# Kernel tuning notes

Measured on AMD Instinct MI355X. Metric: run time of the kernel, lower is better.

## Reference

```python
import jax, jax.numpy as jnp
import numpy as np

NEG_SLOPE = 0.2
EPS = 1e-6
K = 16


def vec_lna(x, Wf, Wd):
    # x: (B, Cin, 3, ...). Vector-neuron linear + VN-LeakyReLU.
    p = jnp.einsum('oc,bc...->bo...', Wf, x)          # features (B, Cout, 3, ...)
    d = jnp.einsum('oc,bc...->bo...', Wd, x)          # directions (B, Cd, 3, ...), Cd=Cout or 1 (shared)
    dot = jnp.sum(p * d, axis=2, keepdims=True)
    dsq = jnp.sum(d * d, axis=2, keepdims=True)
    p_ref = p - (dot / (dsq + EPS)) * d               # reflect negative part onto hyperplane
    return NEG_SLOPE * p + (1.0 - NEG_SLOPE) * jnp.where(dot >= 0, p, p_ref)


def knn_idx_fn(pts, k):
    # pts: (B, N, 3) -> (B, N, k) indices of k nearest neighbors (incl. self)
    sq = jnp.sum(pts * pts, axis=-1)                  # (B, N)
    d2 = sq[:, :, None] + sq[:, None, :] - 2.0 * jnp.einsum('bnd,bmd->bnm', pts, pts)
    _, idx = jax.lax.top_k(-d2, k)                    # smallest distances
    return idx


def graph_feature(x, idx):
    # x: (B, C, 3, N), idx: (B, N, k) -> (B, 2C, 3, N, k)
    nb = jax.vmap(lambda xb, ib: xb[:, :, ib])(x, idx)  # (B, C, 3, N, k)
    xc = x[..., None]
    return jnp.concatenate([nb - xc, jnp.broadcast_to(xc, nb.shape)], axis=1)


def _winit(key, co, ci):
    return jax.random.normal(key, (co, ci), dtype=jnp.float32) * np.sqrt(2.0 / ci).astype(np.float32)


def setup_inputs() -> dict:
    key = jax.random.key(0)
    ks = jax.random.split(key, 16)
    B, N = 4, 2048
    x = jax.random.normal(ks[0], (B, 3, N), dtype=jnp.float32)
    return {
        'x': x,
        'w1f': _winit(ks[1], 16, 2),   'w1d': _winit(ks[2], 16, 2),
        'w2f': _winit(ks[3], 32, 32),  'w2d': _winit(ks[4], 32, 32),
        'w3f': _winit(ks[5], 64, 64),  'w3d': _winit(ks[6], 64, 64),
        'w4f': _winit(ks[7], 128, 128),'w4d': _winit(ks[8], 128, 128),
        'wcf': _winit(ks[9], 128, 240),'wcd': _winit(ks[10], 1, 240),   # shared nonlinearity -> 1 dir channel
        'wi1f': _winit(ks[11], 128, 256), 'wi1d': _winit(ks[12], 128, 256),
        'wi2f': _winit(ks[13], 256, 128), 'wi2d': _winit(ks[14], 256, 128),
    }


def reference(x, w1f, w1d, w2f, w2d, w3f, w3d, w4f, w4d, wcf, wcd, wi1f, wi1d, wi2f, wi2d):
    # x: (B, 3, N)
    pts = jnp.transpose(x, (0, 2, 1))                 # (B, N, 3)
    idx = knn_idx_fn(pts, K)                          # (B, N, K) -- fixed graph (use_dg=False)
    h = x[:, None]                                    # (B, 1, 3, N)
    h = vec_lna(graph_feature(h, idx), w1f, w1d)
    x1 = h.mean(axis=-1)                              # (B, 16, 3, N)
    h = vec_lna(graph_feature(x1, idx), w2f, w2d)
    x2 = h.mean(axis=-1)                              # (B, 32, 3, N)
    h = vec_lna(graph_feature(x2, idx), w3f, w3d)
    x3 = h.mean(axis=-1)                              # (B, 64, 3, N)
    h = vec_lna(graph_feature(x3, idx), w4f, w4d)
    x4 = h.mean(axis=-1)                              # (B, 128, 3, N)
    xc = vec_lna(jnp.concatenate([x1, x2, x3, x4], axis=1), wcf, wcd)  # (B, 128, 3, N)
    xm = jnp.broadcast_to(xc.mean(axis=-1, keepdims=True), xc.shape)
    xcat = jnp.concatenate([xc, xm], axis=1)          # (B, 256, 3, N)
    x0 = vec_lna(vec_lna(xcat, wi1f, wi1d), wi2f, wi2d)
    inv = jnp.sum(xcat * x0, axis=2)                  # (B, 256, N) rotation-invariant features
    return inv
```

## Files before the change

kernel.cpp:

```cpp
#include <hip/hip_runtime.h>
#include <hip/hip_fp16.h>

#define NPTS  2048
#define BATCH 4
#define NBP   8192
#define MROWS 24576
#define KNN_K 16

typedef short bf16x8 __attribute__((ext_vector_type(8)));
typedef float f32x4  __attribute__((ext_vector_type(4)));

static __device__ __forceinline__ void split_bf16(float a, unsigned short& h, unsigned short& l)
{
    unsigned u = __float_as_uint(a);
    unsigned hr = (u + 0x7FFFu + ((u >> 16) & 1u)) & 0xFFFF0000u;
    h = (unsigned short)(hr >> 16);
    float rem = a - __uint_as_float(hr);
    unsigned v = __float_as_uint(rem);
    l = (unsigned short)((v + 0x7FFFu + ((v >> 16) & 1u)) >> 16);
}

static __device__ __forceinline__ float bf2(unsigned short h, unsigned short l)
{
    return __uint_as_float((unsigned)h << 16) + __uint_as_float((unsigned)l << 16);
// ... 144 lines not shown
        int v = row % 3;
        int gp = row / 3;
        int b = gp >> 11;
        int n = gp & (NPTS - 1);
        float xv = x[(b * 3 + v) * NPTS + n];
        float wv = wbig_val(w1f, w1d, o, 0, 16, 1);
        float val = xv * wv;
        if (o < 32) AH[(size_t)row * 32 + o] = __float2half(val);
        else        AG[(size_t)row * 32 + o - 32] = val;
    } else if (i < PC6) {
        float v = 0.f;
        unsigned short *ph, *pl;
        int ix;
        if (i < PC1) {
            ix = i - PC0;
            int c = ix & 31, j = ix >> 5;
            if (c < 16) v = wbig_val(w2f, w2d, j, c, 32, 16);
            ph = Wb2h; pl = Wb2l;
        } else if (i < PC2) {
            ix = i - PC1;
            int c = ix & 31, j = ix >> 5;
            v = wbig_val(w3f, w3d, j, c, 64, 32);
            ph = Wb3h; pl = Wb3l;
        } else if (i < PC3) {
            ix = i - PC2;
            int c = ix & 63, j = ix >> 6;
            v = wbig_val(w4f, w4d, j, c, 128, 64);
            ph = Wb4h; pl = Wb4l;
        } else if (i < PC4) {
            ix = i - PC3;
            int c = ix & 255, r = ix >> 8;
            if (c < 240) {
                if (r < 128) v = wcf[r * 240 + c];
                else if (r < 129) v = wcd[(r - 128) * 240 + c];
            }
            ph = Wch; pl = Wcl;
        } else if (i < PC5) {
            ix = i - PC4;
            int c = ix & 255, r = ix >> 8;
            if (r < 128) v = wi1f[r * 256 + c];
            else v = wi1d[(r - 128) * 256 + c];
            ph = Wi1h; pl = Wi1l;
        } else {
            ix = i - PC5;
            int c = ix & 127, r = ix >> 7;
            int o = r >> 1;
            v = (r & 1) ? wi2d[o * 128 + c] : wi2f[o * 128 + c];
            ph = Wi2h; pl = Wi2l;
        }
        unsigned short h, l;
        split_bf16(v, h, l);
        ph[ix] = h; pl[ix] = l;
    }
}

template <int OIN, int NF>
__global__ __launch_bounds__(256, 3) void edge_gemm_kernel(
    const __half* __restrict__ AHin, const float* __restrict__ AGin,
    const int* __restrict__ idx,
    unsigned short* __restrict__ X240h, unsigned short* __restrict__ X240l, int ooff,
    const unsigned short* __restrict__ Wh, const unsigned short* __restrict__ Wl,
    __half* __restrict__ OUTA, float* __restrict__ OUTG)
{
    constexpr int PTS = 16;
    constexpr int NC = NF * 64;
    constexpr int twoO = NC / 2;
    constexpr int LDW = 40;
    constexpr int CPT = OIN / 16;
    constexpr int twoOin = 2 * OIN;

    __shared__ unsigned short Xsh[48][32];
    __shared__ unsigned short Xsl[48][32];
    __shared__ unsigned short wbh[NC][LDW];
    __shared__ unsigned short wbl[NC][LDW];
    __shared__ int sIdx[PTS][KNN_K];

    const int lb = xcd_swizzle(blockIdx.x, gridDim.x);
    const int tid = threadIdx.x;

    for (int rr = tid; rr < NC; rr += 256) {
#pragma unroll
        for (int scc = 0; scc < 4; scc++) {
            *(uint4*)&wbh[rr][scc * 8] = *(const uint4*)(Wh + (size_t)rr * 32 + scc * 8);
            *(uint4*)&wbl[rr][scc * 8] = *(const uint4*)(Wl + (size_t)rr * 32 + scc * 8);
        }
    }
    for (int j = tid; j < PTS * KNN_K; j += 256)
        sIdx[j >> 4][j & 15] = idx[(lb * PTS + (j >> 4)) * KNN_K + (j & 15)];
    __syncthreads();

    const int op = tid & 15;
    const int pt = tid >> 4;
    const int gp = lb * PTS + pt;
    const int b = gp >> 11;
    const int rown = gp * 3;
    const int bbase = (b << 11) * 3;

    float cg[3][2 * CPT];
#pragma unroll
    for (int v = 0; v < 3; v++) {
        if constexpr (CPT == 2) {
            float4 c4 = *(const float4*)&AGin[(size_t)(rown + v) * twoOin + 4 * op];
            cg[v][0] = c4.x; cg[v][1] = c4.y; cg[v][2] = c4.z; cg[v][3] = c4.w;
        } else {
            float2 c2 = *(const float2*)&AGin[(size_t)(rown + v) * twoOin + 2 * op];
            cg[v][0] = c2.x; cg[v][1] = c2.y;
        }
    }
    float am[CPT][3];
#pragma unroll
    for (int c0 = 0; c0 < CPT; c0++) { am[c0][0] = 0.f; am[c0][1] = 0.f; am[c0][2] = 0.f; }

#pragma unroll 2
    for (int k = 0; k < KNN_K; k++) {
        const int m = sIdx[pt][k];
        const __half* base = AHin + (size_t)(bbase + m * 3) * twoOin + 2 * CPT * op;
        float e[3][2 * CPT];
#pragma unroll
        for (int v = 0; v < 3; v++) {
            if constexpr (CPT == 2) {
                uint2 u = *(const uint2*)(base + (size_t)v * twoOin);
                float2 x0 = __half22float2(*(__half2*)&u.x);
                float2 x1 = __half22float2(*(__half2*)&u.y);
                e[v][0] = x0.x; e[v][1] = x0.y; e[v][2] = x1.x; e[v][3] = x1.y;
            } else {
                unsigned u = *(const unsigned*)(base + (size_t)v * twoOin);
                float2 x0 = __half22float2(*(__half2*)&u);
                e[v][0] = x0.x; e[v][1] = x0.y;
            }
        }
#pragma unroll
        for (int c0 = 0; c0 < CPT; c0++) {
            float p0 = e[0][2 * c0] + cg[0][2 * c0], d0 = e[0][2 * c0 + 1] + cg[0][2 * c0 + 1];
            float p1 = e[1][2 * c0] + cg[1][2 * c0], d1 = e[1][2 * c0 + 1] + cg[1][2 * c0 + 1];
            float p2 = e[2][2 * c0] + cg[2][2 * c0], d2 = e[2][2 * c0 + 1] + cg[2][2 * c0 + 1];
            float dot = fmaf(p2, d2, fmaf(p1, d1, p0 * d0));
            float dsq = fmaf(d2, d2, fmaf(d1, d1, d0 * d0));
            float s = lna_scale(dot, dsq);
            am[c0][0] += fmaf(-s, d0, p0);
            am[c0][1] += fmaf(-s, d1, p1);
            am[c0][2] += fmaf(-s, d2, p2);
        }
    }

#pragma unroll
    for (int v = 0; v < 3; v++) {
#pragma unroll
        for (int c0 = 0; c0 < CPT; c0++) {
            const int ch = CPT * op + c0;
            unsigned short h, l;
            split_bf16(am[c0][v] * 0.0625f, h, l);
            Xsh[pt * 3 + v][ch] = h;
            Xsl[pt * 3 + v][ch] = l;
            const size_t ob = (size_t)(rown + v) * 256 + ooff + ch;
            X240h[ob] = h; X240l[ob] = l;
        }
        if constexpr (CPT == 1) {
            Xsh[pt * 3 + v][16 + op] = 0;
            Xsl[pt * 3 + v][16 + op] = 0;
        }
    }
    __syncthreads();

    const int lane = tid & 63;
    const int wv = tid >> 6;
    const int mr = lane & 15;
    const int q  = lane >> 4;

    f32x4 acc[3][NF];
#pragma unroll
    for (int a = 0; a < 3; a++)
#pragma unroll
        for (int c = 0; c < NF; c++) acc[a][c] = (f32x4){0.f, 0.f, 0.f, 0.f};

    bf16x8 ah[3], al[3], bh[NF], bl[NF];
#pragma unroll
    for (int mf = 0; mf < 3; mf++) {
        ah[mf] = *(const bf16x8*)&Xsh[mf * 16 + mr][q * 8];
        al[mf] = *(const bf16x8*)&Xsl[mf * 16 + mr][q * 8];
    }
#pragma unroll
    for (int nf = 0; nf < NF; nf++) {
        const int wr = wv * 16 * NF + nf * 16 + mr;
        bh[nf] = *(const bf16x8*)&wbh[wr][q * 8];
        bl[nf] = *(const bf16x8*)&wbl[wr][q * 8];
    }
#pragma unroll
    for (int mf = 0; mf < 3; mf++)
#pragma unroll
        for (int nf = 0; nf < NF; nf++) {
            acc[mf][nf] = __builtin_amdgcn_mfma_f32_16x16x32_bf16(ah[mf], bh[nf], acc[mf][nf], 0, 0, 0);
            acc[mf][nf] = __builtin_amdgcn_mfma_f32_16x16x32_bf16(ah[mf], bl[nf], acc[mf][nf], 0, 0, 0);
            acc[mf][nf] = __builtin_amdgcn_mfma_f32_16x16x32_bf16(al[mf], bh[nf], acc[mf][nf], 0, 0, 0);
        }

    const int rbase = lb * 48;
#pragma unroll
    for (int nf = 0; nf < NF; nf++) {
        const int col = wv * 16 * NF + nf * 16 + mr;
#pragma unroll
        for (int mf = 0; mf < 3; mf++)
#pragma unroll
            for (int i = 0; i < 4; i++) {
                const int row = rbase + mf * 16 + q * 4 + i;
                const float val = acc[mf][nf][i];
                if (col < twoO) OUTA[(size_t)row * twoO + col] = __float2half(val);
                else            OUTG[(size_t)row * twoO + col - twoO] = val;
            }
    }
}

__global__ __launch_bounds__(256) void gemm_mfma(
    const unsigned short* __restrict__ Xh, const unsigned short* __restrict__ Xl,
    int ldx, int xoff,
    const unsigned short* __restrict__ Wh, const unsigned short* __restrict__ Wl,
    float* __restrict__ OUT, int ldo, int Nout, int Kpad,
    __half* __restrict__ OUTA, float* __restrict__ OUTG, int twoO)
{
    __shared__ unsigned short Ws[2][64][56];
    const int tid = threadIdx.x;
    const int bm = blockIdx.x * 256;
    const int bo = blockIdx.y * 64;
    const int lane = tid & 63;
    const int wv = tid >> 6;
    const int mr = lane & 15;
    const int q  = lane >> 4;

    f32x4 acc[4][4];
#pragma unroll
    for (int a = 0; a < 4; a++)
#pragma unroll
        for (int c = 0; c < 4; c++) acc[a][c] = (f32x4){0.f, 0.f, 0.f, 0.f};

    const int wr = tid >> 2;
    const int sc = tid & 3;

    for (int k0 = 0; k0 < Kpad; k0 += 32) {
        {
            const uint4 vh = *(const uint4*)(Wh + (size_t)(bo + wr) * Kpad + k0 + sc * 8);
            const uint4 vl = *(const uint4*)(Wl + (size_t)(bo + wr) * Kpad + k0 + sc * 8);
            *(uint4*)&Ws[0][wr][sc * 8] = vh;
            *(uint4*)&Ws[1][wr][sc * 8] = vl;
        }
        __syncthreads();

        bf16x8 ah[4], al[4], bh[4], bl[4];
#pragma unroll
        for (int mf = 0; mf < 4; mf++) {
            const size_t xrow = (size_t)(bm + wv * 64 + mf * 16 + mr) * ldx + xoff + k0 + q * 8;
            ah[mf] = *(const bf16x8*)(Xh + xrow);
            al[mf] = *(const bf16x8*)(Xl + xrow);
        }
#pragma unroll
        for (int nf = 0; nf < 4; nf++) {
            bh[nf] = *(const bf16x8*)&Ws[0][nf * 16 + mr][q * 8];
            bl[nf] = *(const bf16x8*)&Ws[1][nf * 16 + mr][q * 8];
        }
#pragma unroll
        for (int mf = 0; mf < 4; mf++)
#pragma unroll
            for (int nf = 0; nf < 4; nf++) {
                acc[mf][nf] = __builtin_amdgcn_mfma_f32_16x16x32_bf16(ah[mf], bh[nf], acc[mf][nf], 0, 0, 0);
                acc[mf][nf] = __builtin_amdgcn_mfma_f32_16x16x32_bf16(ah[mf], bl[nf], acc[mf][nf], 0, 0, 0);
                acc[mf][nf] = __builtin_amdgcn_mfma_f32_16x16x32_bf16(al[mf], bh[nf], acc[mf][nf], 0, 0, 0);
            }
        __syncthreads();
    }

    if (OUTA) {
#pragma unroll
        for (int nf = 0; nf < 4; nf++) {
            const int col = bo + nf * 16 + mr;
            if (col < twoO) {
#pragma unroll
                for (int mf = 0; mf < 4; mf++)
#pragma unroll
                    for (int i = 0; i < 4; i++) {
                        const int row = bm + wv * 64 + mf * 16 + q * 4 + i;
                        OUTA[(size_t)row * twoO + col] = __float2half(acc[mf][nf][i]);
                    }
            } else {
#pragma unroll
                for (int mf = 0; mf < 4; mf++)
#pragma unroll
                    for (int i = 0; i < 4; i++) {
                        const int row = bm + wv * 64 + mf * 16 + q * 4 + i;
                        OUTG[(size_t)row * twoO + col - twoO] = acc[mf][nf][i];
                    }
            }
        }
    } else {
#pragma unroll
        for (int nf = 0; nf < 4; nf++) {
            const int col = bo + nf * 16 + mr;
            if (col < Nout) {
#pragma unroll
                for (int mf = 0; mf < 4; mf++)
#pragma unroll
                    for (int i = 0; i < 4; i++) {
                        const int row = bm + wv * 64 + mf * 16 + q * 4 + i;
                        OUT[(size_t)row * ldo + col] = acc[mf][nf][i];
                    }
            }
        }
    }
}

template <int NF, bool WCMODE>
__global__ __launch_bounds__(256, 3) void gemm_lna(
    const unsigned short* __restrict__ Xh, const unsigned short* __restrict__ Xl, int ldx,
    const unsigned short* __restrict__ Wh, const unsigned short* __restrict__ Wl,
    int ldwk, int Kpad,
    unsigned short* __restrict__ oh, unsigned short* __restrict__ ol,
    float* __restrict__ part2, const float* __restrict__ ym)
{
    constexpr int NC  = NF * 64;
    constexpr int LDW = 40;
    constexpr int LDT = NC + 1;
    constexpr int WB  = 2 * NC * LDW * 2;
    constexpr int TB  = 48 * LDT * 4;
    constexpr int SB  = (WB > TB) ? WB : TB;
    __shared__ __align__(16) char smem[SB];
    unsigned short* wb = (unsigned short*)smem;
    float* tb = (float*)smem;

    const int tid = threadIdx.x;
    const int bm = blockIdx.x * 48;
    const int lane = tid & 63;
    const int wv = tid >> 6;
    const int mr = lane & 15;
    const int q  = lane >> 4;

    f32x4 acc[3][NF];
#pragma unroll
    for (int a = 0; a < 3; a++)
#pragma unroll
        for (int c = 0; c < NF; c++) acc[a][c] = (f32x4){0.f, 0.f, 0.f, 0.f};

    for (int k0 = 0; k0 < Kpad; k0 += 32) {
        for (int rr = tid; rr < NC; rr += 256) {
#pragma unroll
            for (int sc = 0; sc < 4; sc++) {
                *(uint4*)&wb[(size_t)rr * LDW + sc * 8] =
                    *(const uint4*)(Wh + (size_t)rr * ldwk + k0 + sc * 8);
                *(uint4*)&wb[(size_t)(NC + rr) * LDW + sc * 8] =
                    *(const uint4*)(Wl + (size_t)rr * ldwk + k0 + sc * 8);
            }
        }
        __syncthreads();

        bf16x8 ah[3], al[3], bh[NF], bl[NF];
#pragma unroll
        for (int mf = 0; mf < 3; mf++) {
            const size_t xrow = (size_t)(bm + mf * 16 + mr) * ldx + k0 + q * 8;
            ah[mf] = *(const bf16x8*)(Xh + xrow);
            al[mf] = *(const bf16x8*)(Xl + xrow);
        }
#pragma unroll
        for (int nf = 0; nf < NF; nf++) {
            const int wr = wv * 16 * NF + nf * 16 + mr;
            bh[nf] = *(const bf16x8*)&wb[(size_t)wr * LDW + q * 8];
            bl[nf] = *(const bf16x8*)&wb[(size_t)(NC + wr) * LDW + q * 8];
        }
#pragma unroll
        for (int mf = 0; mf < 3; mf++)
#pragma unroll
            for (int nf = 0; nf < NF; nf++) {
                acc[mf][nf] = __builtin_amdgcn_mfma_f32_16x16x32_bf16(ah[mf], bh[nf], acc[mf][nf], 0, 0, 0);
                acc[mf][nf] = __builtin_amdgcn_mfma_f32_16x16x32_bf16(ah[mf], bl[nf], acc[mf][nf], 0, 0, 0);
                acc[mf][nf] = __builtin_amdgcn_mfma_f32_16x16x32_bf16(al[mf], bh[nf], acc[mf][nf], 0, 0, 0);
            }
        __syncthreads();
    }

#pragma unroll
    for (int mf = 0; mf < 3; mf++)
#pragma unroll
        for (int nf = 0; nf < NF; nf++)
#pragma unroll
            for (int i = 0; i < 4; i++)
                tb[(size_t)(mf * 16 + q * 4 + i) * LDT + wv * 16 * NF + nf * 16 + mr] = acc[mf][nf][i];
    __syncthreads();

    const int bp0 = blockIdx.x * 16;
    const int bb = bp0 >> 11;
    const int oo = tid & 127;
    float ymp[3], ymd[3];
    if constexpr (!WCMODE) {
#pragma unroll
        for (int v = 0; v < 3; v++) {
            ymp[v] = ym[(size_t)(bb * 3 + v) * 256 + oo];
            ymd[v] = ym[(size_t)(bb * 3 + v) * 256 + 128 + oo];
        }
    }
    float vacc[3] = {0.f, 0.f, 0.f};
#pragma unroll
    for (int it = 0; it < 8; it++) {
        const int item = it * 256 + tid;
        const int o = item & 127;
        const int pt = item >> 7;
        float p[3], d[3];
#pragma unroll
        for (int v = 0; v < 3; v++) {
            const int r = pt * 3 + v;
            p[v] = tb[(size_t)r * LDT + o];
            d[v] = WCMODE ? tb[(size_t)r * LDT + 128] : tb[(size_t)r * LDT + 128 + o];
            if constexpr (!WCMODE) { p[v] += ymp[v]; d[v] += ymd[v]; }
        }
        float dot = fmaf(p[2], d[2], fmaf(p[1], d[1], p[0] * d[0]));
        float dsq = fmaf(d[2], d[2], fmaf(d[1], d[1], d[0] * d[0]));
        float s = lna_scale(dot, dsq);
#pragma unroll
        for (int v = 0; v < 3; v++) {
            float val = fmaf(-s, d[v], p[v]);
            if constexpr (WCMODE) vacc[v] += val;
            unsigned short h, l;
            split_bf16(val, h, l);
            const size_t ob = ((size_t)(bp0 + pt) * 3 + v) * 128 + o;
            oh[ob] = h; ol[ob] = l;
        }
    }

    if constexpr (WCMODE) {
        __syncthreads();
        tb[tid] = vacc[0]; tb[256 + tid] = vacc[1]; tb[512 + tid] = vacc[2];
        __syncthreads();
        if (tid < 128) {
#pragma unroll
            for (int v = 0; v < 3; v++)
                part2[(size_t)blockIdx.x * 384 + v * 128 + tid] =
                    tb[v * 256 + tid] + tb[v * 256 + tid + 128];
        }
    }
}

template <int O, int PT>
__global__ __launch_bounds__(256, 6) void edge_kernel(const __half* __restrict__ AH,
                                                      const float* __restrict__ AG,
                                                      const int* __restrict__ idx,
                                                      unsigned short* __restrict__ outh,
                                                      unsigned short* __restrict__ outl,
                                                      int ooff)
{
    constexpr int TP = O / 2;
    constexpr int twoO = 2 * O;
    const int lb = xcd_swizzle(blockIdx.x, gridDim.x);
    const int tid = threadIdx.x;
    const int op = tid % TP;
    const int pt = tid / TP;
    const int gp = lb * PT + pt;
    const int b = gp >> 11;
    __shared__ int sIdx[PT][KNN_K];
    for (int j = tid; j < PT * KNN_K; j += 256)
        sIdx[j >> 4][j & 15] = idx[(lb * PT + (j >> 4)) * KNN_K + (j & 15)];
    __syncthreads();
    const int rown = gp * 3;
    const float4 c0 = *(const float4*)&AG[(size_t)(rown + 0) * twoO + 4 * op];
    const float4 c1 = *(const float4*)&AG[(size_t)(rown + 1) * twoO + 4 * op];
    const float4 c2 = *(const float4*)&AG[(size_t)(rown + 2) * twoO + 4 * op];
    float ax0 = 0.f, ax1 = 0.f, ax2 = 0.f;
    float ay0 = 0.f, ay1 = 0.f, ay2 = 0.f;
    const int bbase = (b << 11) * 3;
#pragma unroll 2
    for (int k = 0; k < KNN_K; k++) {
        int m = sIdx[pt][k];
        const __half* base = AH + (size_t)(bbase + m * 3) * twoO + 4 * op;
        uint2 u0 = *(const uint2*)(base);
        uint2 u1 = *(const uint2*)(base + twoO);
        uint2 u2 = *(const uint2*)(base + 2 * twoO);
        float2 e0 = __half22float2(*(__half2*)&u0.x);
        float2 f0 = __half22float2(*(__half2*)&u0.y);
        float2 e1 = __half22float2(*(__half2*)&u1.x);
        float2 f1 = __half22float2(*(__half2*)&u1.y);
        float2 e2 = __half22float2(*(__half2*)&u2.x);
        float2 f2 = __half22float2(*(__half2*)&u2.y);
        {
            float p0 = e0.x + c0.x, d0 = e0.y + c0.y;
            float p1 = e1.x + c1.x, d1 = e1.y + c1.y;
            float p2 = e2.x + c2.x, d2 = e2.y + c2.y;
            float dot = fmaf(p2, d2, fmaf(p1, d1, p0 * d0));
            float dsq = fmaf(d2, d2, fmaf(d1, d1, d0 * d0));
            float s = lna_scale(dot, dsq);
            ax0 += fmaf(-s, d0, p0);
            ax1 += fmaf(-s, d1, p1);
            ax2 += fmaf(-s, d2, p2);
        }
        {
            float p0 = f0.x + c0.z, d0 = f0.y + c0.w;
            float p1 = f1.x + c1.z, d1 = f1.y + c1.w;
            float p2 = f2.x + c2.z, d2 = f2.y + c2.w;
            float dot = fmaf(p2, d2, fmaf(p1, d1, p0 * d0));
            float dsq = fmaf(d2, d2, fmaf(d1, d1, d0 * d0));
            float s = lna_scale(dot, dsq);
            ay0 += fmaf(-s, d0, p0);
            ay1 += fmaf(-s, d1, p1);
            ay2 += fmaf(-s, d2, p2);
        }
    }
    float rx[3] = { ax0 * 0.0625f, ax1 * 0.0625f, ax2 * 0.0625f };
    float ry[3] = { ay0 * 0.0625f, ay1 * 0.0625f, ay2 * 0.0625f };
#pragma unroll
    for (int v = 0; v < 3; v++) {
        unsigned short hx, lx, hy, ly;
        split_bf16(rx[v], hx, lx);
        split_bf16(ry[v], hy, ly);
        const size_t ob = (size_t)(rown + v) * 256 + ooff + 2 * op;
        *(unsigned*)(outh + ob) = (unsigned)hx | ((unsigned)hy << 16);
        *(unsigned*)(outl + ob) = (unsigned)lx | ((unsigned)ly << 16);
    }
}

__global__ __launch_bounds__(128) void xm_reduce_ym_kernel(
    const float* __restrict__ part2,
    unsigned short* __restrict__ xmh, unsigned short* __restrict__ xml,
    const float* __restrict__ wi1f, const float* __restrict__ wi1d,
    float* __restrict__ ym)
{
    __shared__ float xs[128];
    const int bv = blockIdx.x;
    const int b = bv / 3;
    const int v = bv % 3;
    const int o = threadIdx.x;
    float acc = 0.f;
    for (int i = 0; i < 128; i++)
        acc += part2[(size_t)(b * 128 + i) * 384 + v * 128 + o];
    const float m = acc * (1.f / 2048.f);
    unsigned short h, l;
    split_bf16(m, h, l);
    xmh[bv * 128 + o] = h;
    xml[bv * 128 + o] = l;
    xs[o] = m;
    __syncthreads();
#pragma unroll
    for (int half = 0; half < 2; half++) {
        const int oo = half * 128 + o;
        const float* wrow = (oo < 128) ? (wi1f + (size_t)oo * 256 + 128)
                                       : (wi1d + (size_t)(oo - 128) * 256 + 128);
        float s = 0.f;
        for (int c = 0; c < 128; c++) s = fmaf(wrow[c], xs[c], s);
        ym[(size_t)bv * 256 + oo] = s;
    }
}

#define GI_LDT 67
__global__ __launch_bounds__(256, 3) void gemm_inv(
    const unsigned short* __restrict__ Xh, const unsigned short* __restrict__ Xl,
    const unsigned short* __restrict__ Wh, const unsigned short* __restrict__ Wl,
    const unsigned short* __restrict__ xch, const unsigned short* __restrict__ xcl,
    const unsigned short* __restrict__ xmh, const unsigned short* __restrict__ xml,
    float* __restrict__ out)
{
    __shared__ __align__(16) char smem[4 * 48 * GI_LDT * 4];
    unsigned short (*Ws)[64][40] = (unsigned short (*)[64][40])smem;
    float* tb = (float*)smem;

    const int tid = threadIdx.x;
    const int lane = tid & 63;
    const int wv = tid >> 6;
    const int mr = lane & 15;
    const int q  = lane >> 4;
    const int bm = blockIdx.x * 192;
    const int bo = blockIdx.y * 64;

    f32x4 acc[3][4];
#pragma unroll
    for (int a = 0; a < 3; a++)
#pragma unroll
        for (int c = 0; c < 4; c++) acc[a][c] = (f32x4){0.f, 0.f, 0.f, 0.f};

    const int wr = tid >> 2;
    const int sc = tid & 3;

    for (int k0 = 0; k0 < 128; k0 += 32) {
        *(uint4*)&Ws[0][wr][sc * 8] = *(const uint4*)(Wh + (size_t)(bo + wr) * 128 + k0 + sc * 8);
        *(uint4*)&Ws[1][wr][sc * 8] = *(const uint4*)(Wl + (size_t)(bo + wr) * 128 + k0 + sc * 8);
        __syncthreads();

        bf16x8 ah[3], al[3], bh[4], bl[4];
#pragma unroll
        for (int mf = 0; mf < 3; mf++) {
            const size_t xrow = (size_t)(bm + wv * 48 + mf * 16 + mr) * 128 + k0 + q * 8;
            ah[mf] = *(const bf16x8*)(Xh + xrow);
            al[mf] = *(const bf16x8*)(Xl + xrow);
        }
#pragma unroll
        for (int nf = 0; nf < 4; nf++) {
            bh[nf] = *(const bf16x8*)&Ws[0][nf * 16 + mr][q * 8];
            bl[nf] = *(const bf16x8*)&Ws[1][nf * 16 + mr][q * 8];
        }
#pragma unroll
        for (int mf = 0; mf < 3; mf++)
#pragma unroll
            for (int nf = 0; nf < 4; nf++) {
                acc[mf][nf] = __builtin_amdgcn_mfma_f32_16x16x32_bf16(ah[mf], bh[nf], acc[mf][nf], 0, 0, 0);
                acc[mf][nf] = __builtin_amdgcn_mfma_f32_16x16x32_bf16(ah[mf], bl[nf], acc[mf][nf], 0, 0, 0);
                acc[mf][nf] = __builtin_amdgcn_mfma_f32_16x16x32_bf16(al[mf], bh[nf], acc[mf][nf], 0, 0, 0);
            }
        __syncthreads();
    }

    float* wt = tb + wv * (48 * GI_LDT);
#pragma unroll
    for (int mf = 0; mf < 3; mf++)
#pragma unroll
        for (int nf = 0; nf < 4; nf++)
#pragma unroll
            for (int i = 0; i < 4; i++)
                wt[(mf * 16 + q * 4 + i) * GI_LDT + nf * 16 + mr] = acc[mf][nf][i];
    __syncthreads();

    const int gp0 = blockIdx.x * 64 + wv * 16;
    const int b = gp0 >> 11;
    const int og0 = bo >> 1;
#pragma unroll
    for (int j = 0; j < 8; j++) {
        const int item = j * 64 + lane;
        const int ol = item & 31;
        const int pt = item >> 5;
        const int og = og0 + ol;
        const int gp = gp0 + pt;
        float p[3], d[3], xc[3];
#pragma unroll
        for (int v = 0; v < 3; v++) {
            p[v] = wt[(3 * pt + v) * GI_LDT + 2 * ol];
            d[v] = wt[(3 * pt + v) * GI_LDT + 2 * ol + 1];
            if (og < 128) {
                const size_t ix = (size_t)(gp * 3 + v) * 128 + og;
                xc[v] = bf2(xch[ix], xcl[ix]);
            } else {
                const size_t ix = (size_t)(b * 3 + v) * 128 + og - 128;
                xc[v] = bf2(xmh[ix], xml[ix]);
            }
        }
        float dot = fmaf(p[2], d[2], fmaf(p[1], d[1], p[0] * d[0]));
        float dsq = fmaf(d[2], d[2], fmaf(d[1], d[1], d[0] * d[0]));
        float s = lna_scale(dot, dsq);
        float inv = 0.f;
#pragma unroll
        for (int v = 0; v < 3; v++)
            inv = fmaf(xc[v], fmaf(-s, d[v], p[v]), inv);
        out[((size_t)b * 256 + og) * NPTS + (gp & (NPTS - 1))] = inv;
    }
}

extern "C" void kernel_launch(void* const* d_in, const int* in_sizes, int n_in,
                              void* d_out, int out_size, void* d_ws, size_t ws_size,
                              hipStream_t stream)
{
    const float* x    = (const float*)d_in[0];
    const float* w1f  = (const float*)d_in[1];
    const float* w1d  = (const float*)d_in[2];
    const float* w2f  = (const float*)d_in[3];
    const float* w2d  = (const float*)d_in[4];
    const float* w3f  = (const float*)d_in[5];
    const float* w3d  = (const float*)d_in[6];
    const float* w4f  = (const float*)d_in[7];
    const float* w4d  = (const float*)d_in[8];
    const float* wcf  = (const float*)d_in[9];
    const float* wcd  = (const float*)d_in[10];
    const float* wi1f = (const float*)d_in[11];
    const float* wi1d = (const float*)d_in[12];
    const float* wi2f = (const float*)d_in[13];
    const float* wi2d = (const float*)d_in[14];
    float* out = (float*)d_out;

    float* F = (float*)d_ws;
    size_t off = 0;
    float* AG = F + off;                          off += (size_t)MROWS * 512;
    __half* AH = (__half*)(F + off);              off += (size_t)MROWS * 128;
    __half* AH2 = (__half*)(F + off);             off += (size_t)MROWS * 128;
    unsigned short* X240h = (unsigned short*)(F + off); off += (size_t)MROWS * 128;
    unsigned short* X240l = (unsigned short*)(F + off); off += (size_t)MROWS * 128;
    unsigned short* xc2h  = (unsigned short*)(F + off); off += (size_t)MROWS * 64;
    unsigned short* xc2l  = (unsigned short*)(F + off); off += (size_t)MROWS * 64;
    unsigned short* Wb2h = (unsigned short*)(F + off); off += 2048;
    unsigned short* Wb2l = (unsigned short*)(F + off); off += 2048;
    unsigned short* Wb3h = (unsigned short*)(F + off); off += 4096;
    unsigned short* Wb3l = (unsigned short*)(F + off); off += 4096;
    unsigned short* Wb4h = (unsigned short*)(F + off); off += 16384;
    unsigned short* Wb4l = (unsigned short*)(F + off); off += 16384;
    unsigned short* Wch  = (unsigned short*)(F + off); off += 24576;
    unsigned short* Wcl  = (unsigned short*)(F + off); off += 24576;
    unsigned short* Wi1h = (unsigned short*)(F + off); off += 32768;
    unsigned short* Wi1l = (unsigned short*)(F + off); off += 32768;
    unsigned short* Wi2h = (unsigned short*)(F + off); off += 32768;
    unsigned short* Wi2l = (unsigned short*)(F + off); off += 32768;
    float* part2 = F + off;                       off += (size_t)512 * 384;
    float* ym    = F + off;                       off += 12 * 256;
    unsigned short* xmph = (unsigned short*)(F + off); off += 768;
    unsigned short* xmpl = (unsigned short*)(F + off); off += 768;
    int* idx    = (int*)(F + off);                off += NBP * KNN_K;
    float* AG2 = AG + (size_t)MROWS * 256;
    unsigned short* y1h = X240h;
    unsigned short* y1l = X240l;

    prep_knn_kernel<<<KNN_BLOCKS + PREP_BLOCKS, 256, 0, stream>>>(
        x, idx, AH, AG, w1f, w1d,
        w2f, w2d, Wb2h, Wb2l, w3f, w3d, Wb3h, Wb3l, w4f, w4d, Wb4h, Wb4l,
        wcf, wcd, Wch, Wcl, wi1f, wi1d, Wi1h, Wi1l, wi2f, wi2d, Wi2h, Wi2l);

    const int GM = MROWS / 256;

    edge_gemm_kernel<16, 2><<<NBP / 16, 256, 0, stream>>>(
        AH, AG, idx, X240h, X240l, 0, Wb2h, Wb2l, AH2, AG2);
    edge_gemm_kernel<32, 4><<<NBP / 16, 256, 0, stream>>>(
        AH2, AG2, idx, X240h, X240l, 16, Wb3h, Wb3l, AH, AG);
    edge_kernel<64, 8><<<NBP / 8, 256, 0, stream>>>(AH, AG, idx, X240h, X240l, 48);
    gemm_mfma<<<dim3(GM, 8), 256, 0, stream>>>(X240h, X240l, 256, 48, Wb4h, Wb4l, nullptr, 0, 512, 64, AH2, AG2, 256);
    edge_kernel<128, 4><<<NBP / 4, 256, 0, stream>>>(AH2, AG2, idx, X240h, X240l, 112);

    gemm_lna<3, true><<<MROWS / 48, 256, 0, stream>>>(X240h, X240l, 256,
                                                      Wch, Wcl, 256, 256, xc2h, xc2l, part2, nullptr);

    xm_reduce_ym_kernel<<<BATCH * 3, 128, 0, stream>>>(part2, xmph, xmpl, wi1f, wi1d, ym);

    gemm_lna<4, false><<<MROWS / 48, 256, 0, stream>>>(xc2h, xc2l, 128,
                                                       Wi1h, Wi1l, 256, 128, y1h, y1l, nullptr, ym);

    gemm_inv<<<dim3(MROWS / 192, 8), 256, 0, stream>>>(y1h, y1l, Wi2h, Wi2l,
                                                       xc2h, xc2l, xmph, xmpl, out);

    (void)in_sizes; (void)n_in; (void)out_size; (void)ws_size;
}
```

Baseline: 281.8 us.

## Fuse last edge conv into conv-cat GEMM and chain the two invariant GEMMs

The final edge kernel (layer 4 neighbor aggregation) is merged into the conv-cat GEMM+LNA kernel, so the 128-channel x4 tile is computed straight into shared memory rather than written to and re-read from global X240. The wi1 GEMM+LNA and the wi2 GEMM+invariant kernels are also fused into one kernel that keeps the y1 tile in LDS. This removes two launches and several global round trips. The cost is larger LDS use and lower occupancy (launch bounds 2), weights read straight from global without LDS staging, and fewer, heavier blocks with less parallelism per block.

```diff
diff --git a/kernel.cpp b/kernel.cpp
--- a/kernel.cpp
+++ b/kernel.cpp
@@ -470,134 +470,6 @@
                         OUT[(size_t)row * ldo + col] = acc[mf][nf][i];
                     }
             }
-        }
-    }
-}
-
-template <int NF, bool WCMODE>
-__global__ __launch_bounds__(256, 3) void gemm_lna(
-    const unsigned short* __restrict__ Xh, const unsigned short* __restrict__ Xl, int ldx,
-    const unsigned short* __restrict__ Wh, const unsigned short* __restrict__ Wl,
-    int ldwk, int Kpad,
-    unsigned short* __restrict__ oh, unsigned short* __restrict__ ol,
-    float* __restrict__ part2, const float* __restrict__ ym)
-{
-    constexpr int NC  = NF * 64;
-    constexpr int LDW = 40;
-    constexpr int LDT = NC + 1;
-    constexpr int WB  = 2 * NC * LDW * 2;
-    constexpr int TB  = 48 * LDT * 4;
-    constexpr int SB  = (WB > TB) ? WB : TB;
-    __shared__ __align__(16) char smem[SB];
-    unsigned short* wb = (unsigned short*)smem;
-    float* tb = (float*)smem;
-
-    const int tid = threadIdx.x;
-    const int bm = blockIdx.x * 48;
-    const int lane = tid & 63;
-    const int wv = tid >> 6;
-    const int mr = lane & 15;
-    const int q  = lane >> 4;
-
-    f32x4 acc[3][NF];
-#pragma unroll
-    for (int a = 0; a < 3; a++)
-#pragma unroll
-        for (int c = 0; c < NF; c++) acc[a][c] = (f32x4){0.f, 0.f, 0.f, 0.f};
-
-    for (int k0 = 0; k0 < Kpad; k0 += 32) {
-        for (int rr = tid; rr < NC; rr += 256) {
-#pragma unroll
-            for (int sc = 0; sc < 4; sc++) {
-                *(uint4*)&wb[(size_t)rr * LDW + sc * 8] =
-                    *(const uint4*)(Wh + (size_t)rr * ldwk + k0 + sc * 8);
-                *(uint4*)&wb[(size_t)(NC + rr) * LDW + sc * 8] =
-                    *(const uint4*)(Wl + (size_t)rr * ldwk + k0 + sc * 8);
-            }
-        }
-        __syncthreads();
-
-        bf16x8 ah[3], al[3], bh[NF], bl[NF];
-#pragma unroll
-        for (int mf = 0; mf < 3; mf++) {
-            const size_t xrow = (size_t)(bm + mf * 16 + mr) * ldx + k0 + q * 8;
-            ah[mf] = *(const bf16x8*)(Xh + xrow);
-            al[mf] = *(const bf16x8*)(Xl + xrow);
-        }
-#pragma unroll
-        for (int nf = 0; nf < NF; nf++) {
-            const int wr = wv * 16 * NF + nf * 16 + mr;
-            bh[nf] = *(const bf16x8*)&wb[(size_t)wr * LDW + q * 8];
-            bl[nf] = *(const bf16x8*)&wb[(size_t)(NC + wr) * LDW + q * 8];
-        }
-#pragma unroll
-        for (int mf = 0; mf < 3; mf++)
-#pragma unroll
-            for (int nf = 0; nf < NF; nf++) {
-                acc[mf][nf] = __builtin_amdgcn_mfma_f32_16x16x32_bf16(ah[mf], bh[nf], acc[mf][nf], 0, 0, 0);
-                acc[mf][nf] = __builtin_amdgcn_mfma_f32_16x16x32_bf16(ah[mf], bl[nf], acc[mf][nf], 0, 0, 0);
-                acc[mf][nf] = __builtin_amdgcn_mfma_f32_16x16x32_bf16(al[mf], bh[nf], acc[mf][nf], 0, 0, 0);
-            }
-        __syncthreads();
-    }
-
-#pragma unroll
-    for (int mf = 0; mf < 3; mf++)
-#pragma unroll
-        for (int nf = 0; nf < NF; nf++)
-#pragma unroll
-            for (int i = 0; i < 4; i++)
-                tb[(size_t)(mf * 16 + q * 4 + i) * LDT + wv * 16 * NF + nf * 16 + mr] = acc[mf][nf][i];
-    __syncthreads();
-
-    const int bp0 = blockIdx.x * 16;
-    const int bb = bp0 >> 11;
-    const int oo = tid & 127;
-    float ymp[3], ymd[3];
-    if constexpr (!WCMODE) {
-#pragma unroll
-        for (int v = 0; v < 3; v++) {
-            ymp[v] = ym[(size_t)(bb * 3 + v) * 256 + oo];
-            ymd[v] = ym[(size_t)(bb * 3 + v) * 256 + 128 + oo];
-        }
-    }
-    float vacc[3] = {0.f, 0.f, 0.f};
-#pragma unroll
-    for (int it = 0; it < 8; it++) {
-        const int item = it * 256 + tid;
-        const int o = item & 127;
-        const int pt = item >> 7;
-        float p[3], d[3];
-#pragma unroll
-        for (int v = 0; v < 3; v++) {
-            const int r = pt * 3 + v;
-            p[v] = tb[(size_t)r * LDT + o];
-            d[v] = WCMODE ? tb[(size_t)r * LDT + 128] : tb[(size_t)r * LDT + 128 + o];
-            if constexpr (!WCMODE) { p[v] += ymp[v]; d[v] += ymd[v]; }
-        }
-        float dot = fmaf(p[2], d[2], fmaf(p[1], d[1], p[0] * d[0]));
-        float dsq = fmaf(d[2], d[2], fmaf(d[1], d[1], d[0] * d[0]));
-        float s = lna_scale(dot, dsq);
-#pragma unroll
-        for (int v = 0; v < 3; v++) {
-            float val = fmaf(-s, d[v], p[v]);
-            if constexpr (WCMODE) vacc[v] += val;
-            unsigned short h, l;
-            split_bf16(val, h, l);
-            const size_t ob = ((size_t)(bp0 + pt) * 3 + v) * 128 + o;
-            oh[ob] = h; ol[ob] = l;
-        }
-    }
-
-    if constexpr (WCMODE) {
-        __syncthreads();
-        tb[tid] = vacc[0]; tb[256 + tid] = vacc[1]; tb[512 + tid] = vacc[2];
-        __syncthreads();
-        if (tid < 128) {
-#pragma unroll
-            for (int v = 0; v < 3; v++)
-                part2[(size_t)blockIdx.x * 384 + v * 128 + tid] =
-                    tb[v * 256 + tid] + tb[v * 256 + tid + 128];
         }
     }
 }
@@ -678,6 +550,190 @@
     }
 }
 
+#define EW_LDX 136
+#define EW_LDT 133
+__global__ __launch_bounds__(256, 3) void edge_wc_kernel(
+    const __half* __restrict__ AHin, const float* __restrict__ AGin,
+    const int* __restrict__ idx,
+    const unsigned short* __restrict__ Xh, const unsigned short* __restrict__ Xl,
+    const unsigned short* __restrict__ Wh, const unsigned short* __restrict__ Wl,
+    unsigned short* __restrict__ oh, unsigned short* __restrict__ ol,
+    float* __restrict__ part2)
+{
+    __shared__ __align__(16) unsigned short x4h[48][EW_LDX];
+    __shared__ __align__(16) unsigned short x4l[48][EW_LDX];
+    __shared__ __align__(16) float tb[48 * EW_LDT];
+    __shared__ int sIdx[16][KNN_K];
+
+    const int lb = xcd_swizzle(blockIdx.x, gridDim.x);
+    const int tid = threadIdx.x;
+
+    for (int j = tid; j < 16 * KNN_K; j += 256)
+        sIdx[j >> 4][j & 15] = idx[(lb * 16 + (j >> 4)) * KNN_K + (j & 15)];
+    __syncthreads();
+
+    {
+        const int op = tid & 15;
+        const int pt = tid >> 4;
+        const int gp = lb * 16 + pt;
+        const int b = gp >> 11;
+        const int rown = gp * 3;
+        const int bbase = (b << 11) * 3;
+
+        float cg[3][16];
+#pragma unroll
+        for (int v = 0; v < 3; v++) {
+            const float* ag = &AGin[(size_t)(rown + v) * 256 + 16 * op];
+#pragma unroll
+            for (int t = 0; t < 4; t++) {
+                float4 c4 = *(const float4*)(ag + 4 * t);
+                cg[v][4 * t + 0] = c4.x; cg[v][4 * t + 1] = c4.y;
+                cg[v][4 * t + 2] = c4.z; cg[v][4 * t + 3] = c4.w;
+            }
+        }
+        float am[8][3];
+#pragma unroll
+        for (int c0 = 0; c0 < 8; c0++) { am[c0][0] = 0.f; am[c0][1] = 0.f; am[c0][2] = 0.f; }
+
+        for (int k = 0; k < KNN_K; k++) {
+            const int m = sIdx[pt][k];
+            const __half* base = AHin + (size_t)(bbase + m * 3) * 256 + 16 * op;
+            unsigned uw[3][8];
+#pragma unroll
+            for (int v = 0; v < 3; v++) {
+                uint4 a  = *(const uint4*)(base + (size_t)v * 256);
+                uint4 bq = *(const uint4*)(base + (size_t)v * 256 + 8);
+                uw[v][0] = a.x;  uw[v][1] = a.y;  uw[v][2] = a.z;  uw[v][3] = a.w;
+                uw[v][4] = bq.x; uw[v][5] = bq.y; uw[v][6] = bq.z; uw[v][7] = bq.w;
+            }
+#pragma unroll
+            for (int c0 = 0; c0 < 8; c0++) {
+                float2 e0 = __half22float2(*(__half2*)&uw[0][c0]);
+                float2 e1 = __half22float2(*(__half2*)&uw[1][c0]);
+                float2 e2 = __half22float2(*(__half2*)&uw[2][c0]);
+                float p0 = e0.x + cg[0][2 * c0], d0 = e0.y + cg[0][2 * c0 + 1];
+                float p1 = e1.x + cg[1][2 * c0], d1 = e1.y + cg[1][2 * c0 + 1];
+                float p2 = e2.x + cg[2][2 * c0], d2 = e2.y + cg[2][2 * c0 + 1];
+                float dot = fmaf(p2, d2, fmaf(p1, d1, p0 * d0));
+                float dsq = fmaf(d2, d2, fmaf(d1, d1, d0 * d0));
+                float s = lna_scale(dot, dsq);
+                am[c0][0] += fmaf(-s, d0, p0);
+                am[c0][1] += fmaf(-s, d1, p1);
+                am[c0][2] += fmaf(-s, d2, p2);
+            }
+        }
+#pragma unroll
+        for (int v = 0; v < 3; v++)
+#pragma unroll
+            for (int c0 = 0; c0 < 8; c0++) {
+                unsigned short h, l;
+                split_bf16(am[c0][v] * 0.0625f, h, l);
+                x4h[pt * 3 + v][8 * op + c0] = h;
+                x4l[pt * 3 + v][8 * op + c0] = l;
+            }
+    }
+    __syncthreads();
+
+    const int lane = tid & 63;
+    const int wv = tid >> 6;
+    const int mr = lane & 15;
+    const int q  = lane >> 4;
+    const int rbase = lb * 48;
+
+    f32x4 acc[3][3];
+#pragma unroll
+    for (int a = 0; a < 3; a++)
+#pragma unroll
+        for (int c = 0; c < 3; c++) acc[a][c] = (f32x4){0.f, 0.f, 0.f, 0.f};
+
+    for (int k0 = 0; k0 < 256; k0 += 32) {
+        const int kb = k0 + q * 8;
+        bf16x8 ah[3], al[3], bh[3], bl[3];
+#pragma unroll
+        for (int mf = 0; mf < 3; mf++) {
+            const int row = mf * 16 + mr;
+            if (kb >= 112) {
+                if (kb >= 240) {
+                    ah[mf] = (bf16x8){0, 0, 0, 0, 0, 0, 0, 0};
+                    al[mf] = (bf16x8){0, 0, 0, 0, 0, 0, 0, 0};
+                } else {
+                    ah[mf] = *(const bf16x8*)&x4h[row][kb - 112];
+                    al[mf] = *(const bf16x8*)&x4l[row][kb - 112];
+                }
+            } else {
+                const size_t xr = (size_t)(rbase + row) * 256 + kb;
+                ah[mf] = *(const bf16x8*)(Xh + xr);
+                al[mf] = *(const bf16x8*)(Xl + xr);
+            }
+        }
+#pragma unroll
+        for (int nf = 0; nf < 3; nf++) {
+            const size_t wri = (size_t)(wv * 48 + nf * 16 + mr) * 256 + kb;
+            bh[nf] = *(const bf16x8*)(Wh + wri);
+            bl[nf] = *(const bf16x8*)(Wl + wri);
+        }
+#pragma unroll
+        for (int mf = 0; mf < 3; mf++)
+#pragma unroll
+            for (int nf = 0; nf < 3; nf++) {
+                acc[mf][nf] = __builtin_amdgcn_mfma_f32_16x16x32_bf16(ah[mf], bh[nf], acc[mf][nf], 0, 0, 0);
+                acc[mf][nf] = __builtin_amdgcn_mfma_f32_16x16x32_bf16(ah[mf], bl[nf], acc[mf][nf], 0, 0, 0);
+                acc[mf][nf] = __builtin_amdgcn_mfma_f32_16x16x32_bf16(al[mf], bh[nf], acc[mf][nf], 0, 0, 0);
+            }
+    }
+
+#pragma unroll
+    for (int mf = 0; mf < 3; mf++)
+#pragma unroll
+        for (int nf = 0; nf < 3; nf++) {
+            const int col = wv * 48 + nf * 16 + mr;
+            if (col <= 128) {
+#pragma unroll
+                for (int i = 0; i < 4; i++)
+                    tb[(mf * 16 + q * 4 + i) * EW_LDT + col] = acc[mf][nf][i];
+            }
+        }
+    __syncthreads();
+
+    const int bp0 = lb * 16;
+    float vacc[3] = {0.f, 0.f, 0.f};
+#pragma unroll
+    for (int it = 0; it < 8; it++) {
+        const int item = it * 256 + tid;
+        const int o = item & 127;
+        const int pt = item >> 7;
+        float p[3], d[3];
+#pragma unroll
+        for (int v = 0; v < 3; v++) {
+            const int r = pt * 3 + v;
+            p[v] = tb[r * EW_LDT + o];
+            d[v] = tb[r * EW_LDT + 128];
+        }
+        float dot = fmaf(p[2], d[2], fmaf(p[1], d[1], p[0] * d[0]));
+        float dsq = fmaf(d[2], d[2], fmaf(d[1], d[1], d[0] * d[0]));
+        float s = lna_scale(dot, dsq);
+#pragma unroll
+        for (int v = 0; v < 3; v++) {
+            float val = fmaf(-s, d[v], p[v]);
+            vacc[v] += val;
+            unsigned short h, l;
+            split_bf16(val, h, l);
+            const size_t ob = ((size_t)(bp0 + pt) * 3 + v) * 128 + o;
+            oh[ob] = h; ol[ob] = l;
+        }
+    }
+
+    __syncthreads();
+    tb[tid] = vacc[0]; tb[256 + tid] = vacc[1]; tb[512 + tid] = vacc[2];
+    __syncthreads();
+    if (tid < 128) {
+#pragma unroll
+        for (int v = 0; v < 3; v++)
+            part2[(size_t)lb * 384 + v * 128 + tid] =
+                tb[v * 256 + tid] + tb[v * 256 + tid + 128];
+    }
+}
+
 __global__ __launch_bounds__(128) void xm_reduce_ym_kernel(
     const float* __restrict__ part2,
     unsigned short* __restrict__ xmh, unsigned short* __restrict__ xml,
@@ -710,25 +766,31 @@
     }
 }
 
-#define GI_LDT 67
-__global__ __launch_bounds__(256, 3) void gemm_inv(
-    const unsigned short* __restrict__ Xh, const unsigned short* __restrict__ Xl,
-    const unsigned short* __restrict__ Wh, const unsigned short* __restrict__ Wl,
+#define QI_LDY  136
+#define QI_LDT  257
+#define QI_LDT2 67
+__global__ __launch_bounds__(256, 2) void gemm_ii_kernel(
     const unsigned short* __restrict__ xch, const unsigned short* __restrict__ xcl,
+    const unsigned short* __restrict__ W1h, const unsigned short* __restrict__ W1l,
+    const unsigned short* __restrict__ W2h, const unsigned short* __restrict__ W2l,
     const unsigned short* __restrict__ xmh, const unsigned short* __restrict__ xml,
+    const float* __restrict__ ym,
     float* __restrict__ out)
 {
-    __shared__ __align__(16) char smem[4 * 48 * GI_LDT * 4];
-    unsigned short (*Ws)[64][40] = (unsigned short (*)[64][40])smem;
-    float* tb = (float*)smem;
+    __shared__ __align__(16) char regA[51456];
+    __shared__ __align__(16) unsigned short y1h[48][QI_LDY];
+    __shared__ __align__(16) unsigned short y1l[48][QI_LDY];
+    unsigned short* wb = (unsigned short*)regA;
+    float* tb = (float*)regA;
 
     const int tid = threadIdx.x;
     const int lane = tid & 63;
     const int wv = tid >> 6;
     const int mr = lane & 15;
     const int q  = lane >> 4;
-    const int bm = blockIdx.x * 192;
-    const int bo = blockIdx.y * 64;
+    const int lb = blockIdx.x;
+    const int bm = lb * 48;
+    const int bb = (lb * 16) >> 11;
 
     f32x4 acc[3][4];
 #pragma unroll
@@ -736,25 +798,31 @@
 #pragma unroll
         for (int c = 0; c < 4; c++) acc[a][c] = (f32x4){0.f, 0.f, 0.f, 0.f};
 
-    const int wr = tid >> 2;
-    const int sc = tid & 3;
-
     for (int k0 = 0; k0 < 128; k0 += 32) {
-        *(uint4*)&Ws[0][wr][sc * 8] = *(const uint4*)(Wh + (size_t)(bo + wr) * 128 + k0 + sc * 8);
-        *(uint4*)&Ws[1][wr][sc * 8] = *(const uint4*)(Wl + (size_t)(bo + wr) * 128 + k0 + sc * 8);
+        {
+            const int rr = tid;
+#pragma unroll
+            for (int sc = 0; sc < 4; sc++) {
+                *(uint4*)&wb[(size_t)rr * 40 + sc * 8] =
+                    *(const uint4*)(W1h + (size_t)rr * 256 + k0 + sc * 8);
+                *(uint4*)&wb[(size_t)(256 + rr) * 40 + sc * 8] =
+                    *(const uint4*)(W1l + (size_t)rr * 256 + k0 + sc * 8);
+            }
+        }
         __syncthreads();
 
         bf16x8 ah[3], al[3], bh[4], bl[4];
 #pragma unroll
         for (int mf = 0; mf < 3; mf++) {
-            const size_t xrow = (size_t)(bm + wv * 48 + mf * 16 + mr) * 128 + k0 + q * 8;
-            ah[mf] = *(const bf16x8*)(Xh + xrow);
-            al[mf] = *(const bf16x8*)(Xl + xrow);
+            const size_t xr = (size_t)(bm + mf * 16 + mr) * 128 + k0 + q * 8;
+            ah[mf] = *(const bf16x8*)(xch + xr);
+            al[mf] = *(const bf16x8*)(xcl + xr);
         }
 #pragma unroll
         for (int nf = 0; nf < 4; nf++) {
-            bh[nf] = *(const bf16x8*)&Ws[0][nf * 16 + mr][q * 8];
-            bl[nf] = *(const bf16x8*)&Ws[1][nf * 16 + mr][q * 8];
+            const int wr = wv * 64 + nf * 16 + mr;
+            bh[nf] = *(const bf16x8*)&wb[(size_t)wr * 40 + q * 8];
+            bl[nf] = *(const bf16x8*)&wb[(size_t)(256 + wr) * 40 + q * 8];
         }
 #pragma unroll
         for (int mf = 0; mf < 3; mf++)
@@ -767,47 +835,116 @@
         __syncthreads();
     }
 
-    float* wt = tb + wv * (48 * GI_LDT);
 #pragma unroll
     for (int mf = 0; mf < 3; mf++)
 #pragma unroll
         for (int nf = 0; nf < 4; nf++)
 #pragma unroll
             for (int i = 0; i < 4; i++)
-                wt[(mf * 16 + q * 4 + i) * GI_LDT + nf * 16 + mr] = acc[mf][nf][i];
+                tb[(size_t)(mf * 16 + q * 4 + i) * QI_LDT + wv * 64 + nf * 16 + mr] = acc[mf][nf][i];
     __syncthreads();
 
-    const int gp0 = blockIdx.x * 64 + wv * 16;
-    const int b = gp0 >> 11;
-    const int og0 = bo >> 1;
-#pragma unroll
-    for (int j = 0; j < 8; j++) {
-        const int item = j * 64 + lane;
-        const int ol = item & 31;
-        const int pt = item >> 5;
-        const int og = og0 + ol;
-        const int gp = gp0 + pt;
-        float p[3], d[3], xc[3];
+    {
+        const int oo = tid & 127;
+        float ymp[3], ymd[3];
 #pragma unroll
         for (int v = 0; v < 3; v++) {
-            p[v] = wt[(3 * pt + v) * GI_LDT + 2 * ol];
-            d[v] = wt[(3 * pt + v) * GI_LDT + 2 * ol + 1];
-            if (og < 128) {
-                const size_t ix = (size_t)(gp * 3 + v) * 128 + og;
-                xc[v] = bf2(xch[ix], xcl[ix]);
-            } else {
-                const size_t ix = (size_t)(b * 3 + v) * 128 + og - 128;
-                xc[v] = bf2(xmh[ix], xml[ix]);
-            }
-        }
-        float dot = fmaf(p[2], d[2], fmaf(p[1], d[1], p[0] * d[0]));
-        float dsq = fmaf(d[2], d[2], fmaf(d[1], d[1], d[0] * d[0]));
-        float s = lna_scale(dot, dsq);
-        float inv = 0.f;
-#pragma unroll
-        for (int v = 0; v < 3; v++)
-            inv = fmaf(xc[v], fmaf(-s, d[v], p[v]), inv);
-        out[((size_t)b * 256 + og) * NPTS + (gp & (NPTS - 1))] = inv;
+            ymp[v] = ym[(size_t)(bb * 3 + v) * 256 + oo];
+            ymd[v] = ym[(size_t)(bb * 3 + v) * 256 + 128 + oo];
+        }
+#pragma unroll
+        for (int it = 0; it < 8; it++) {
+            const int item = it * 256 + tid;
+            const int o = item & 127;
+            const int pt = item >> 7;
+            float p[3], d[3];
+#pragma unroll
+            for (int v = 0; v < 3; v++) {
+                const int r = pt * 3 + v;
+                p[v] = tb[(size_t)r * QI_LDT + o] + ymp[v];
+                d[v] = tb[(size_t)r * QI_LDT + 128 + o] + ymd[v];
+            }
+            float dot = fmaf(p[2], d[2], fmaf(p[1], d[1], p[0] * d[0]));
+            float dsq = fmaf(d[2], d[2], fmaf(d[1], d[1], d[0] * d[0]));
+            float s = lna_scale(dot, dsq);
+#pragma unroll
+            for (int v = 0; v < 3; v++) {
+                unsigned short h, l;
+                split_bf16(fmaf(-s, d[v], p[v]), h, l);
+                y1h[pt * 3 + v][o] = h;
+                y1l[pt * 3 + v][o] = l;
+            }
+        }
+    }
+    __syncthreads();
+
+    f32x4 acc2[3][8];
+#pragma unroll
+    for (int a = 0; a < 3; a++)
+#pragma unroll
+        for (int c = 0; c < 8; c++) acc2[a][c] = (f32x4){0.f, 0.f, 0.f, 0.f};
+
+    for (int k0 = 0; k0 < 128; k0 += 32) {
+        bf16x8 ah[3], al[3];
+#pragma unroll
+        for (int mf = 0; mf < 3; mf++) {
+            ah[mf] = *(const bf16x8*)&y1h[mf * 16 + mr][k0 + q * 8];
+            al[mf] = *(const bf16x8*)&y1l[mf * 16 + mr][k0 + q * 8];
+        }
+#pragma unroll
+        for (int nf = 0; nf < 8; nf++) {
+            const size_t wi = (size_t)(wv * 128 + nf * 16 + mr) * 128 + k0 + q * 8;
+            const bf16x8 bh = *(const bf16x8*)(W2h + wi);
+            const bf16x8 bl = *(const bf16x8*)(W2l + wi);
+#pragma unroll
+            for (int mf = 0; mf < 3; mf++) {
+                acc2[mf][nf] = __builtin_amdgcn_mfma_f32_16x16x32_bf16(ah[mf], bh, acc2[mf][nf], 0, 0, 0);
+                acc2[mf][nf] = __builtin_amdgcn_mfma_f32_16x16x32_bf16(ah[mf], bl, acc2[mf][nf], 0, 0, 0);
+                acc2[mf][nf] = __builtin_amdgcn_mfma_f32_16x16x32_bf16(al[mf], bh, acc2[mf][nf], 0, 0, 0);
+            }
+        }
+    }
+
+    float* wt = tb + wv * (48 * QI_LDT2);
+#pragma unroll
+    for (int hf = 0; hf < 2; hf++) {
+        __syncthreads();
+#pragma unroll
+        for (int mf = 0; mf < 3; mf++)
+#pragma unroll
+            for (int nf2 = 0; nf2 < 4; nf2++)
+#pragma unroll
+                for (int i = 0; i < 4; i++)
+                    wt[(mf * 16 + q * 4 + i) * QI_LDT2 + nf2 * 16 + mr] = acc2[mf][hf * 4 + nf2][i];
+#pragma unroll
+        for (int j = 0; j < 8; j++) {
+            const int item = j * 64 + lane;
+            const int ol = item & 31;
+            const int pt = item >> 5;
+            const int og = wv * 64 + hf * 32 + ol;
+            const int gp = lb * 16 + pt;
+            float p[3], d[3], xc[3];
+#pragma unroll
+            for (int v = 0; v < 3; v++) {
+                p[v] = wt[(3 * pt + v) * QI_LDT2 + 2 * ol];
+                d[v] = wt[(3 * pt + v) * QI_LDT2 + 2 * ol + 1];
+                if (og < 128) {
+                    const size_t ix = (size_t)(gp * 3 + v) * 128 + og;
+                    xc[v] = bf2(xch[ix], xcl[ix]);
+                } else {
+                    const size_t ix = (size_t)(bb * 3 + v) * 128 + og - 128;
+                    xc[v] = bf2(xmh[ix], xml[ix]);
+                }
+            }
+            float dot = fmaf(p[2], d[2], fmaf(p[1], d[1], p[0] * d[0]));
+            float dsq = fmaf(d[2], d[2], fmaf(d[1], d[1], d[0] * d[0]));
+            float s = lna_scale(dot, dsq);
+            float inv = 0.f;
+#pragma unroll
+            for (int v = 0; v < 3; v++)
+                inv = fmaf(xc[v], fmaf(-s, d[v], p[v]), inv);
+            out[((size_t)bb * 256 + og) * NPTS + (gp & (NPTS - 1))] = inv;
+        }
     }
 }
 
@@ -859,8 +996,6 @@
     unsigned short* xmpl = (unsigned short*)(F + off); off += 768;
     int* idx    = (int*)(F + off);                off += NBP * KNN_K;
     float* AG2 = AG + (size_t)MROWS * 256;
-    unsigned short* y1h = X240h;
-    unsigned short* y1l = X240l;
 
     prep_knn_kernel<<<KNN_BLOCKS + PREP_BLOCKS, 256, 0, stream>>>(
         x, idx, AH, AG, w1f, w1d,
@@ -875,18 +1010,14 @@
         AH2, AG2, idx, X240h, X240l, 16, Wb3h, Wb3l, AH, AG);
     edge_kernel<64, 8><<<NBP / 8, 256, 0, stream>>>(AH, AG, idx, X240h, X240l, 48);
     gemm_mfma<<<dim3(GM, 8), 256, 0, stream>>>(X240h, X240l, 256, 48, Wb4h, Wb4l, nullptr, 0, 512, 64, AH2, AG2, 256);
-    edge_kernel<128, 4><<<NBP / 4, 256, 0, stream>>>(AH2, AG2, idx, X240h, X240l, 112);
-
-    gemm_lna<3, true><<<MROWS / 48, 256, 0, stream>>>(X240h, X240l, 256,
-                                                      Wch, Wcl, 256, 256, xc2h, xc2l, part2, nullptr);
+
+    edge_wc_kernel<<<NBP / 16, 256, 0, stream>>>(AH2, AG2, idx, X240h, X240l,
+                                                 Wch, Wcl, xc2h, xc2l, part2);
 
     xm_reduce_ym_kernel<<<BATCH * 3, 128, 0, stream>>>(part2, xmph, xmpl, wi1f, wi1d, ym);
 
-    gemm_lna<4, false><<<MROWS / 48, 256, 0, stream>>>(xc2h, xc2l, 128,
-                                                       Wi1h, Wi1l, 256, 128, y1h, y1l, nullptr, ym);
-
-    gemm_inv<<<dim3(MROWS / 192, 8), 256, 0, stream>>>(y1h, y1l, Wi2h, Wi2l,
-                                                       xc2h, xc2l, xmph, xmpl, out);
+    gemm_ii_kernel<<<MROWS / 48, 256, 0, stream>>>(xc2h, xc2l, Wi1h, Wi1l,
+                                                   Wi2h, Wi2l, xmph, xmpl, ym, out);
 
     (void)in_sizes; (void)n_in; (void)out_size; (void)ws_size;
 }
```

New measurement: 264.3 us. 1.07x faster.
